# Kernel tuning notes

Measured on AMD Instinct MI355X. Metric: run time of the kernel, lower is better.

Reference implementation:

```python
import jax, jax.numpy as jnp
import numpy as np


def setup_inputs() -> dict:
    key = jax.random.key(0)
    ks = jax.random.split(key, 8)
    B, N, F = 16, 2048, 128
    x = jax.random.normal(ks[0], (B, N, F), dtype=jnp.float32)
    # dense (pre-normalized) adjacency, as spektral GCNConv expects normalized A
    a = jax.random.uniform(ks[1], (B, N, N), dtype=jnp.float32) / N
    w1 = jax.random.normal(ks[2], (F, 32), dtype=jnp.float32) * 0.1
    b1 = jnp.zeros((32,), dtype=jnp.float32)
    w2 = jax.random.normal(ks[3], (32, 32), dtype=jnp.float32) * 0.1
    b2 = jnp.zeros((32,), dtype=jnp.float32)
    wf1 = jax.random.normal(ks[4], (32, 512), dtype=jnp.float32) * 0.1
    bf1 = jnp.zeros((512,), dtype=jnp.float32)
    wf2 = jax.random.normal(ks[5], (512, 1), dtype=jnp.float32) * 0.1
    bf2 = jnp.zeros((1,), dtype=jnp.float32)
    return {"x": x, "a": a, "w1": w1, "b1": b1, "w2": w2, "b2": b2,
            "wf1": wf1, "bf1": bf1, "wf2": wf2, "bf2": bf2}


def _gcn(x, a, w, b):
    # GCNConv: elu(A_norm @ X @ W + b)
    h = jnp.einsum('bnf,fc->bnc', x, w)   # dense transform first (cheaper)
    h = jnp.einsum('bnm,bmc->bnc', a, h)  # adjacency aggregation
    return jax.nn.elu(h + b)


def reference(x, a, w1, b1, w2, b2, wf1, bf1, wf2, bf2):
    h = _gcn(x, a, w1, b1)                # [B,N,32]
    h = _gcn(h, a, w2, b2)                # [B,N,32]
    pooled = jnp.sum(h, axis=1)           # GlobalSumPool -> [B,32]
    h = jax.nn.relu(pooled @ wf1 + bf1)   # [B,512]
    out = jax.nn.sigmoid(h @ wf2 + bf2)   # [B,1]
    return out
```

## Files before the change

### kernel.cpp

```cpp
#include <hip/hip_runtime.h>
#include <hip/hip_bf16.h>
#include <math.h>

#define BATCH 16
#define NN 2048
#define FF 128
#define CC 32
#define HID 512
#define QM 512
#define LSTR 520

typedef float v4f __attribute__((ext_vector_type(4)));
typedef short short8 __attribute__((ext_vector_type(8)));

__device__ __forceinline__ unsigned short f2bf(float f) {
  unsigned u = __float_as_uint(f);
  u += 0x7fffu + ((u >> 16) & 1u);
  return (unsigned short)(u >> 16);
}

__device__ __forceinline__ float elu1(float x) {
  return x > 0.f ? x : expm1f(x);
}

__global__ __launch_bounds__(256)
void k_xw1(const float* __restrict__ src, const float* __restrict__ w,
           unsigned short* __restrict__ outT) {
  int t = threadIdx.x;
  int wv = t >> 6, l = t & 63, lo = l & 15, q = l >> 4;
  int rowt = blockIdx.x * 4 + wv;
  long row = (long)rowt * 16 + lo;

  short8 wf[FF / 32][2];
#pragma unroll
  for (int kc = 0; kc < FF / 32; ++kc)
#pragma unroll
    for (int h = 0; h < 2; ++h) {
      short8 f;
#pragma unroll
      for (int j = 0; j < 8; ++j)
        f[j] = (short)f2bf(w[(kc * 32 + q * 8 + j) * CC + h * 16 + lo]);
      wf[kc][h] = f;
    }

  v4f acc0 = {0.f, 0.f, 0.f, 0.f}, acc1 = {0.f, 0.f, 0.f, 0.f};
#pragma unroll
  for (int kc = 0; kc < FF / 32; ++kc) {
    const float* sp = src + row * FF + kc * 32 + q * 8;
    float4 a0 = *(const float4*)sp;
    float4 a1 = *(const float4*)(sp + 4);
    short8 af;
    af[0] = (short)f2bf(a0.x); af[1] = (short)f2bf(a0.y);
    af[2] = (short)f2bf(a0.z); af[3] = (short)f2bf(a0.w);
    af[4] = (short)f2bf(a1.x); af[5] = (short)f2bf(a1.y);
    af[6] = (short)f2bf(a1.z); af[7] = (short)f2bf(a1.w);
    acc0 = __builtin_amdgcn_mfma_f32_16x16x32_bf16(af, wf[kc][0], acc0, 0, 0, 0);
    acc1 = __builtin_amdgcn_mfma_f32_16x16x32_bf16(af, wf[kc][1], acc1, 0, 0, 0);
  }

  int b = rowt >> 7;
  int nbase = (rowt & 127) * 16;
#pragma unroll
  for (int r = 0; r < 4; ++r) {
    int n = nbase + q * 4 + r;
    outT[((long)b * CC + lo) * NN + n] = f2bf(acc0[r]);
    outT[((long)b * CC + 16 + lo) * NN + n] = f2bf(acc1[r]);
  }
}

__global__ __launch_bounds__(256, 4)
void k_agg1(const float* __restrict__ a,
            unsigned short* __restrict__ abf,
            const unsigned short* __restrict__ hT,
            float* __restrict__ hpart) {
  __shared__ unsigned short hs[CC * LSTR];

  int t = threadIdx.x;
  int bid = blockIdx.x;
  int rt = bid & 31, qm = (bid >> 5) & 3, b = bid >> 7;

#pragma unroll
  for (int i = 0; i < 8; ++i) {
    int j = i * 256 + t;
    int c = j >> 6, off = (j & 63) * 8;
    uint4 v = *(const uint4*)(hT + ((long)b * CC + c) * NN + qm * QM + off);
    *(uint4*)&hs[c * LSTR + off] = v;
  }
  __syncthreads();

  int wv = t >> 6, l = t & 63, lo = l & 15, q = l >> 4;
  int n0 = rt * 64 + wv * 16;
  long abase = ((long)(b * NN + n0 + lo)) * NN + qm * QM + q * 8;
  const float* arow = a + abase;
  unsigned short* aout = abf + abase;
  const unsigned short* h0 = &hs[lo * LSTR + q * 8];

  v4f acc0 = {0.f, 0.f, 0.f, 0.f}, acc1 = {0.f, 0.f, 0.f, 0.f};
#pragma unroll
  for (int mm = 0; mm < QM; mm += 32) {
    float4 a0 = *(const float4*)(arow + mm);
    float4 a1 = *(const float4*)(arow + mm + 4);
    short8 af;
    af[0] = (short)f2bf(a0.x); af[1] = (short)f2bf(a0.y);
    af[2] = (short)f2bf(a0.z); af[3] = (short)f2bf(a0.w);
    af[4] = (short)f2bf(a1.x); af[5] = (short)f2bf(a1.y);
    af[6] = (short)f2bf(a1.z); af[7] = (short)f2bf(a1.w);
    *(short8*)(aout + mm) = af;
    short8 b0 = *(const short8*)(h0 + mm);
    short8 b1 = *(const short8*)(h0 + 16 * LSTR + mm);
    acc0 = __builtin_amdgcn_mfma_f32_16x16x32_bf16(af, b0, acc0, 0, 0, 0);
    acc1 = __builtin_amdgcn_mfma_f32_16x16x32_bf16(af, b1, acc1, 0, 0, 0);
  }

  float* op = hpart + ((long)qm * BATCH * NN + (long)b * NN) * CC;
#pragma unroll
  for (int r = 0; r < 4; ++r) {
    int n = n0 + q * 4 + r;
    op[(long)n * CC + lo] = acc0[r];
    op[(long)n * CC + 16 + lo] = acc1[r];
  }
}

__global__ __launch_bounds__(256, 4)
void k_agg2(const unsigned short* __restrict__ abf,
            const unsigned short* __restrict__ hT,
            float* __restrict__ hpart) {
  __shared__ unsigned short hs[CC * LSTR];

  int t = threadIdx.x;
  int bid = blockIdx.x;
  int rt = bid & 31, qm = (bid >> 5) & 3, b = bid >> 7;

#pragma unroll
  for (int i = 0; i < 8; ++i) {
    int j = i * 256 + t;
    int c = j >> 6, off = (j & 63) * 8;
    uint4 v = *(const uint4*)(hT + ((long)b * CC + c) * NN + qm * QM + off);
    *(uint4*)&hs[c * LSTR + off] = v;
  }
  __syncthreads();

  int wv = t >> 6, l = t & 63, lo = l & 15, q = l >> 4;
  int n0 = rt * 64 + wv * 16;
  const unsigned short* arow =
      abf + ((long)(b * NN + n0 + lo)) * NN + qm * QM + q * 8;
  const unsigned short* h0 = &hs[lo * LSTR + q * 8];

  v4f acc0 = {0.f, 0.f, 0.f, 0.f}, acc1 = {0.f, 0.f, 0.f, 0.f};
#pragma unroll
  for (int mm = 0; mm < QM; mm += 32) {
    short8 af = *(const short8*)(arow + mm);
    short8 b0 = *(const short8*)(h0 + mm);
    short8 b1 = *(const short8*)(h0 + 16 * LSTR + mm);
    acc0 = __builtin_amdgcn_mfma_f32_16x16x32_bf16(af, b0, acc0, 0, 0, 0);
    acc1 = __builtin_amdgcn_mfma_f32_16x16x32_bf16(af, b1, acc1, 0, 0, 0);
  }

  float* op = hpart + ((long)qm * BATCH * NN + (long)b * NN) * CC;
#pragma unroll
  for (int r = 0; r < 4; ++r) {
    int n = n0 + q * 4 + r;
    op[(long)n * CC + lo] = acc0[r];
    op[(long)n * CC + 16 + lo] = acc1[r];
  }
}

__global__ __launch_bounds__(256)
void k_xw2(const float* __restrict__ h1p, const float* __restrict__ b1,
           const float* __restrict__ w2, unsigned short* __restrict__ outT) {
  const long QS = (long)BATCH * NN * CC;
  int t = threadIdx.x;
  int wv = t >> 6, l = t & 63, lo = l & 15, q = l >> 4;
  int rowt = blockIdx.x * 4 + wv;
  long row = (long)rowt * 16 + lo;

  short8 wf[2];
#pragma unroll
  for (int h = 0; h < 2; ++h) {
    short8 f;
#pragma unroll
    for (int j = 0; j < 8; ++j)
      f[j] = (short)f2bf(w2[(q * 8 + j) * CC + h * 16 + lo]);
    wf[h] = f;
  }

  const float* p = h1p + row * CC + q * 8;
  float s[8] = {0, 0, 0, 0, 0, 0, 0, 0};
#pragma unroll
  for (int qq = 0; qq < 4; ++qq) {
    float4 u0 = *(const float4*)(p + qq * QS);
    float4 u1 = *(const float4*)(p + qq * QS + 4);
    s[0] += u0.x; s[1] += u0.y; s[2] += u0.z; s[3] += u0.w;
    s[4] += u1.x; s[5] += u1.y; s[6] += u1.z; s[7] += u1.w;
  }
  short8 af;
#pragma unroll
  for (int j = 0; j < 8; ++j)
    af[j] = (short)f2bf(elu1(s[j] + b1[q * 8 + j]));

  v4f acc0 = {0.f, 0.f, 0.f, 0.f}, acc1 = {0.f, 0.f, 0.f, 0.f};
  acc0 = __builtin_amdgcn_mfma_f32_16x16x32_bf16(af, wf[0], acc0, 0, 0, 0);
  acc1 = __builtin_amdgcn_mfma_f32_16x16x32_bf16(af, wf[1], acc1, 0, 0, 0);

  int b = rowt >> 7;
  int nbase = (rowt & 127) * 16;
#pragma unroll
  for (int r = 0; r < 4; ++r) {
    int n = nbase + q * 4 + r;
    outT[((long)b * CC + lo) * NN + n] = f2bf(acc0[r]);
    outT[((long)b * CC + 16 + lo) * NN + n] = f2bf(acc1[r]);
  }
}

__global__ __launch_bounds__(256)
void k_pool(const float* __restrict__ h2p, const float* __restrict__ b2,
            float* __restrict__ pooled) {
  const long QS = (long)BATCH * NN * CC;
  __shared__ float red[8][CC + 1];
  int t = threadIdx.x;
  int b = blockIdx.x >> 3, seg = blockIdx.x & 7;
  int c = t & 31, nl = t >> 5;
  float bc = b2[c];
  float s = 0.f;
  for (int n = seg * 256 + nl; n < seg * 256 + 256; n += 8) {
    long idx = ((long)b * NN + n) * CC + c;
    s += elu1(h2p[idx] + h2p[QS + idx] + h2p[2 * QS + idx] + h2p[3 * QS + idx] + bc);
  }
  red[nl][c] = s;
  __syncthreads();
  if (nl < 4) red[nl][c] += red[nl + 4][c];
  __syncthreads();
  if (nl < 2) red[nl][c] += red[nl + 2][c];
  __syncthreads();
  if (nl == 0) atomicAdd(&pooled[b * CC + c], red[0][c] + red[1][c]);
}

__global__ __launch_bounds__(512)
void k5_mlp(const float* __restrict__ pooled, const float* __restrict__ wf1,
            const float* __restrict__ bf1, const float* __restrict__ wf2,
            const float* __restrict__ bf2, float* __restrict__ out) {
  __shared__ float red[HID];
  __shared__ float ps[CC];
  int b = blockIdx.x, j = threadIdx.x;
  if (j < CC) ps[j] = pooled[b * CC + j];
  __syncthreads();
  float acc = bf1[j];
#pragma unroll
  for (int c = 0; c < CC; ++c) acc += ps[c] * wf1[c * HID + j];
  red[j] = fmaxf(acc, 0.f) * wf2[j];
  __syncthreads();
  for (int s = HID / 2; s > 0; s >>= 1) {
    if (j < s) red[j] += red[j + s];
    __syncthreads();
  }
  if (j == 0) out[b] = 1.f / (1.f + expf(-(red[0] + bf2[0])));
}

extern "C" void kernel_launch(void* const* d_in, const int* in_sizes, int n_in,
                              void* d_out, int out_size, void* d_ws, size_t ws_size,
                              hipStream_t stream) {
  const float* x   = (const float*)d_in[0];
  const float* a   = (const float*)d_in[1];
  const float* w1  = (const float*)d_in[2];
  const float* b1  = (const float*)d_in[3];
  const float* w2  = (const float*)d_in[4];
  const float* b2  = (const float*)d_in[5];
  const float* wf1 = (const float*)d_in[6];
  const float* bf1 = (const float*)d_in[7];
  const float* wf2 = (const float*)d_in[8];
  const float* bf2 = (const float*)d_in[9];
  float* out = (float*)d_out;

  char* ws = (char*)d_ws;
  unsigned short* abf = (unsigned short*)ws;
  unsigned short* hT1 = (unsigned short*)(ws + 0x8000000UL);
  unsigned short* hT2 = (unsigned short*)(ws + 0x8200000UL);
  float* h1p = (float*)(ws + 0x8400000UL);
  float* h2p = (float*)(ws + 0x9400000UL);
  float* pooled = (float*)(ws + 0xA400000UL);

  hipMemsetAsync(pooled, 0, BATCH * CC * sizeof(float), stream);

  k_xw1<<<512, 256, 0, stream>>>(x, w1, hT1);
  k_agg1<<<2048, 256, 0, stream>>>(a, abf, hT1, h1p);
  k_xw2<<<512, 256, 0, stream>>>(h1p, b1, w2, hT2);
  k_agg2<<<2048, 256, 0, stream>>>(abf, hT2, h2p);
  k_pool<<<128, 256, 0, stream>>>(h2p, b2, pooled);
  k5_mlp<<<BATCH, HID, 0, stream>>>(pooled, wf1, bf1, wf2, bf2, out);
}
```

Baseline: 460.4 us.

## Store scaled FP8 adjacency copy for second aggregation and drop pooled memset

The first aggregation now writes the adjacency intermediate as FP8 scaled by 1024 instead of BF16. This halves the bytes written in agg1 and read back in agg2. The second layer's XW output is divided by 1024 to cancel the scale. agg2 converts FP8 to float and then to BF16 before the MFMA, which adds ALU work. Pool now writes per-segment partial sums that the MLP kernel reduces, replacing atomics and the memset. FP8 quantization of A loses accuracy and could exceed tolerance.

```diff
diff --git a/kernel.cpp b/kernel.cpp
--- a/kernel.cpp
+++ b/kernel.cpp
@@ -11,6 +11,7 @@
 #define LSTR 520
 
 typedef float v4f __attribute__((ext_vector_type(4)));
+typedef float v2f __attribute__((ext_vector_type(2)));
 typedef short short8 __attribute__((ext_vector_type(8)));
 
 __device__ __forceinline__ unsigned short f2bf(float f) {
@@ -69,10 +70,8 @@
 }
 
 __global__ __launch_bounds__(256, 4)
-void k_agg1(const float* __restrict__ a,
-            unsigned short* __restrict__ abf,
-            const unsigned short* __restrict__ hT,
-            float* __restrict__ hpart) {
+void k_agg1(const float* __restrict__ a, unsigned char* __restrict__ afp8,
+            const unsigned short* __restrict__ hT, float* __restrict__ hpart) {
   __shared__ unsigned short hs[CC * LSTR];
 
   int t = threadIdx.x;
@@ -83,8 +82,8 @@
   for (int i = 0; i < 8; ++i) {
     int j = i * 256 + t;
     int c = j >> 6, off = (j & 63) * 8;
-    uint4 v = *(const uint4*)(hT + ((long)b * CC + c) * NN + qm * QM + off);
-    *(uint4*)&hs[c * LSTR + off] = v;
+    *(uint4*)&hs[c * LSTR + off] =
+        *(const uint4*)(hT + ((long)b * CC + c) * NN + qm * QM + off);
   }
   __syncthreads();
 
@@ -92,7 +91,7 @@
   int n0 = rt * 64 + wv * 16;
   long abase = ((long)(b * NN + n0 + lo)) * NN + qm * QM + q * 8;
   const float* arow = a + abase;
-  unsigned short* aout = abf + abase;
+  unsigned char* aout = afp8 + abase;
   const unsigned short* h0 = &hs[lo * LSTR + q * 8];
 
   v4f acc0 = {0.f, 0.f, 0.f, 0.f}, acc1 = {0.f, 0.f, 0.f, 0.f};
@@ -105,51 +104,12 @@
     af[2] = (short)f2bf(a0.z); af[3] = (short)f2bf(a0.w);
     af[4] = (short)f2bf(a1.x); af[5] = (short)f2bf(a1.y);
     af[6] = (short)f2bf(a1.z); af[7] = (short)f2bf(a1.w);
-    *(short8*)(aout + mm) = af;
-    short8 b0 = *(const short8*)(h0 + mm);
-    short8 b1 = *(const short8*)(h0 + 16 * LSTR + mm);
-    acc0 = __builtin_amdgcn_mfma_f32_16x16x32_bf16(af, b0, acc0, 0, 0, 0);
-    acc1 = __builtin_amdgcn_mfma_f32_16x16x32_bf16(af, b1, acc1, 0, 0, 0);
-  }
-
-  float* op = hpart + ((long)qm * BATCH * NN + (long)b * NN) * CC;
-#pragma unroll
-  for (int r = 0; r < 4; ++r) {
-    int n = n0 + q * 4 + r;
-    op[(long)n * CC + lo] = acc0[r];
-    op[(long)n * CC + 16 + lo] = acc1[r];
-  }
-}
-
-__global__ __launch_bounds__(256, 4)
-void k_agg2(const unsigned short* __restrict__ abf,
-            const unsigned short* __restrict__ hT,
-            float* __restrict__ hpart) {
-  __shared__ unsigned short hs[CC * LSTR];
-
-  int t = threadIdx.x;
-  int bid = blockIdx.x;
-  int rt = bid & 31, qm = (bid >> 5) & 3, b = bid >> 7;
-
-#pragma unroll
-  for (int i = 0; i < 8; ++i) {
-    int j = i * 256 + t;
-    int c = j >> 6, off = (j & 63) * 8;
-    uint4 v = *(const uint4*)(hT + ((long)b * CC + c) * NN + qm * QM + off);
-    *(uint4*)&hs[c * LSTR + off] = v;
-  }
-  __syncthreads();
-
-  int wv = t >> 6, l = t & 63, lo = l & 15, q = l >> 4;
-  int n0 = rt * 64 + wv * 16;
-  const unsigned short* arow =
-      abf + ((long)(b * NN + n0 + lo)) * NN + qm * QM + q * 8;
-  const unsigned short* h0 = &hs[lo * LSTR + q * 8];
-
-  v4f acc0 = {0.f, 0.f, 0.f, 0.f}, acc1 = {0.f, 0.f, 0.f, 0.f};
-#pragma unroll
-  for (int mm = 0; mm < QM; mm += 32) {
-    short8 af = *(const short8*)(arow + mm);
+    const float sc = 1024.f;
+    int w0 = __builtin_amdgcn_cvt_pk_fp8_f32(a0.x * sc, a0.y * sc, 0, false);
+    w0 = __builtin_amdgcn_cvt_pk_fp8_f32(a0.z * sc, a0.w * sc, w0, true);
+    int w1 = __builtin_amdgcn_cvt_pk_fp8_f32(a1.x * sc, a1.y * sc, 0, false);
+    w1 = __builtin_amdgcn_cvt_pk_fp8_f32(a1.z * sc, a1.w * sc, w1, true);
+    *(int2*)(aout + mm) = make_int2(w0, w1);
     short8 b0 = *(const short8*)(h0 + mm);
     short8 b1 = *(const short8*)(h0 + 16 * LSTR + mm);
     acc0 = __builtin_amdgcn_mfma_f32_16x16x32_bf16(af, b0, acc0, 0, 0, 0);
@@ -202,19 +162,72 @@
   acc0 = __builtin_amdgcn_mfma_f32_16x16x32_bf16(af, wf[0], acc0, 0, 0, 0);
   acc1 = __builtin_amdgcn_mfma_f32_16x16x32_bf16(af, wf[1], acc1, 0, 0, 0);
 
+  const float inv = 1.f / 1024.f;
   int b = rowt >> 7;
   int nbase = (rowt & 127) * 16;
 #pragma unroll
   for (int r = 0; r < 4; ++r) {
     int n = nbase + q * 4 + r;
-    outT[((long)b * CC + lo) * NN + n] = f2bf(acc0[r]);
-    outT[((long)b * CC + 16 + lo) * NN + n] = f2bf(acc1[r]);
+    outT[((long)b * CC + lo) * NN + n] = f2bf(acc0[r] * inv);
+    outT[((long)b * CC + 16 + lo) * NN + n] = f2bf(acc1[r] * inv);
+  }
+}
+
+__global__ __launch_bounds__(256, 4)
+void k_agg2(const unsigned char* __restrict__ afp8,
+            const unsigned short* __restrict__ hT, float* __restrict__ hpart) {
+  __shared__ unsigned short hs[CC * LSTR];
+
+  int t = threadIdx.x;
+  int bid = blockIdx.x;
+  int rt = bid & 31, qm = (bid >> 5) & 3, b = bid >> 7;
+
+#pragma unroll
+  for (int i = 0; i < 8; ++i) {
+    int j = i * 256 + t;
+    int c = j >> 6, off = (j & 63) * 8;
+    *(uint4*)&hs[c * LSTR + off] =
+        *(const uint4*)(hT + ((long)b * CC + c) * NN + qm * QM + off);
+  }
+  __syncthreads();
+
+  int wv = t >> 6, l = t & 63, lo = l & 15, q = l >> 4;
+  int n0 = rt * 64 + wv * 16;
+  const unsigned char* arow =
+      afp8 + ((long)(b * NN + n0 + lo)) * NN + qm * QM + q * 8;
+  const unsigned short* h0 = &hs[lo * LSTR + q * 8];
+
+  v4f acc0 = {0.f, 0.f, 0.f, 0.f}, acc1 = {0.f, 0.f, 0.f, 0.f};
+#pragma unroll
+  for (int mm = 0; mm < QM; mm += 32) {
+    int2 av = *(const int2*)(arow + mm);
+    v2f f01 = __builtin_amdgcn_cvt_pk_f32_fp8(av.x, false);
+    v2f f23 = __builtin_amdgcn_cvt_pk_f32_fp8(av.x, true);
+    v2f f45 = __builtin_amdgcn_cvt_pk_f32_fp8(av.y, false);
+    v2f f67 = __builtin_amdgcn_cvt_pk_f32_fp8(av.y, true);
+    short8 af;
+    af[0] = (short)f2bf(f01.x); af[1] = (short)f2bf(f01.y);
+    af[2] = (short)f2bf(f23.x); af[3] = (short)f2bf(f23.y);
+    af[4] = (short)f2bf(f45.x); af[5] = (short)f2bf(f45.y);
+    af[6] = (short)f2bf(f67.x); af[7] = (short)f2bf(f67.y);
+    short8 b0 = *(const short8*)(h0 + mm);
+    short8 b1 = *(const short8*)(h0 + 16 * LSTR + mm);
+    acc0 = __builtin_amdgcn_mfma_f32_16x16x32_bf16(af, b0, acc0, 0, 0, 0);
+    acc1 = __builtin_amdgcn_mfma_f32_16x16x32_bf16(af, b1, acc1, 0, 0, 0);
+  }
+
+  float* op = hpart + ((long)qm * BATCH * NN + (long)b * NN) * CC;
+#pragma unroll
+  for (int r = 0; r < 4; ++r) {
+    int n = n0 + q * 4 + r;
+    op[(long)n * CC + lo] = acc0[r];
+    op[(long)n * CC + 16 + lo] = acc1[r];
   }
 }
 
 __global__ __launch_bounds__(256)
 void k_pool(const float* __restrict__ h2p, const float* __restrict__ b2,
-            float* __restrict__ pooled) {
+            float* __restrict__ pp) {
   const long QS = (long)BATCH * NN * CC;
   __shared__ float red[8][CC + 1];
   int t = threadIdx.x;
@@ -232,17 +245,22 @@
   __syncthreads();
   if (nl < 2) red[nl][c] += red[nl + 2][c];
   __syncthreads();
-  if (nl == 0) atomicAdd(&pooled[b * CC + c], red[0][c] + red[1][c]);
+  if (nl == 0) pp[((long)seg * BATCH + b) * CC + c] = red[0][c] + red[1][c];
 }
 
 __global__ __launch_bounds__(512)
-void k5_mlp(const float* __restrict__ pooled, const float* __restrict__ wf1,
+void k5_mlp(const float* __restrict__ pp, const float* __restrict__ wf1,
             const float* __restrict__ bf1, const float* __restrict__ wf2,
             const float* __restrict__ bf2, float* __restrict__ out) {
   __shared__ float red[HID];
   __shared__ float ps[CC];
   int b = blockIdx.x, j = threadIdx.x;
-  if (j < CC) ps[j] = pooled[b * CC + j];
+  if (j < CC) {
+    float s = 0.f;
+#pragma unroll
+    for (int g = 0; g < 8; ++g) s += pp[((long)g * BATCH + b) * CC + j];
+    ps[j] = s;
+  }
   __syncthreads();
   float acc = bf1[j];
 #pragma unroll
@@ -272,19 +290,17 @@
   float* out = (float*)d_out;
 
   char* ws = (char*)d_ws;
-  unsigned short* abf = (unsigned short*)ws;
-  unsigned short* hT1 = (unsigned short*)(ws + 0x8000000UL);
-  unsigned short* hT2 = (unsigned short*)(ws + 0x8200000UL);
-  float* h1p = (float*)(ws + 0x8400000UL);
-  float* h2p = (float*)(ws + 0x9400000UL);
-  float* pooled = (float*)(ws + 0xA400000UL);
-
-  hipMemsetAsync(pooled, 0, BATCH * CC * sizeof(float), stream);
+  unsigned char*  afp8 = (unsigned char*)ws;
+  unsigned short* hT1  = (unsigned short*)(ws + 0x4000000UL);
+  unsigned short* hT2  = (unsigned short*)(ws + 0x4200000UL);
+  float* h1p = (float*)(ws + 0x4400000UL);
+  float* h2p = (float*)(ws + 0x5400000UL);
+  float* pp  = (float*)(ws + 0x6400000UL);
 
   k_xw1<<<512, 256, 0, stream>>>(x, w1, hT1);
-  k_agg1<<<2048, 256, 0, stream>>>(a, abf, hT1, h1p);
+  k_agg1<<<2048, 256, 0, stream>>>(a, afp8, hT1, h1p);
   k_xw2<<<512, 256, 0, stream>>>(h1p, b1, w2, hT2);
-  k_agg2<<<2048, 256, 0, stream>>>(abf, hT2, h2p);
-  k_pool<<<128, 256, 0, stream>>>(h2p, b2, pooled);
-  k5_mlp<<<BATCH, HID, 0, stream>>>(pooled, wf1, bf1, wf2, bf2, out);
-}
+  k_agg2<<<2048, 256, 0, stream>>>(afp8, hT2, h2p);
+  k_pool<<<128, 256, 0, stream>>>(h2p, b2, pp);
+  k5_mlp<<<BATCH, HID, 0, stream>>>(pp, wf1, bf1, wf2, bf2, out);
+}
```

After: 446.6 us. 1.03x faster.
